# Kernel optimization log

Measured on AMD Instinct MI355X. Metric: run time of the kernel, lower is better.

The kernel has to match this reference:

```python
import jax, jax.numpy as jnp
import numpy as np

H = 8          # n_heads
THRESH = 0.5   # edge pruning threshold
LN_EPS = 1e-5


def setup_inputs() -> dict:
    key = jax.random.key(0)
    ks = jax.random.split(key, 24)
    B, S, D = 8, 128, 256
    N = S + 1
    hd = D // H

    def lin(k, fan_in, fan_out, gain=1.0):
        # xavier_uniform-ish init, stored as [in, out] (y = x @ W + b)
        lim = gain * np.sqrt(6.0 / (fan_in + fan_out))
        return jax.random.uniform(k, (fan_in, fan_out), jnp.float32, -lim, lim)

    g = 1.0 / np.sqrt(2.0)
    return {
        "desc": jax.random.normal(ks[0], (B, S, D), jnp.float32),
        "nv": jax.random.normal(ks[1], (B, N, D), jnp.float32),
        "W_gt": lin(ks[2], D, D), "b_gt": jnp.zeros((D,), jnp.float32),
        "topo_bias": jnp.zeros((1,), jnp.float32),
        "W_q": lin(ks[3], D, D, g), "b_q": jnp.zeros((D,), jnp.float32),
        "W_k": lin(ks[4], D, D, g), "b_k": jnp.zeros((D,), jnp.float32),
        "W_v": lin(ks[5], D, D, g), "b_v": jnp.zeros((D,), jnp.float32),
        "W_e1": lin(ks[6], 2 * D, D), "b_e1": jnp.zeros((D,), jnp.float32),
        "ln_g": jnp.ones((D,), jnp.float32), "ln_b": jnp.zeros((D,), jnp.float32),
        "W_e2": lin(ks[7], D, D), "b_e2": jnp.zeros((D,), jnp.float32),
        "w_attn": lin(ks[8], 3 * hd, 1, g)[:, 0], "b_attn": jnp.zeros((), jnp.float32),
        "W_o": lin(ks[9], D, D, g), "b_o": jnp.zeros((D,), jnp.float32),
    }


def _forward(desc, nv, W_gt, b_gt, topo_bias, W_q, b_q, W_k, b_k, W_v, b_v,
             W_e1, b_e1, ln_g, ln_b, W_e2, b_e2, w_attn, b_attn, W_o, b_o):
    B, N, D = nv.shape
    S = N - 1
    hd = D // H

    # 1. global topology
    d = desc @ W_gt + b_gt                                   # [B,S,D]
    dn = d / jnp.linalg.norm(d, axis=-1, keepdims=True)
    global_top = jax.nn.sigmoid(jnp.einsum('bid,bjd->bij', dn, dn) + topo_bias[0])

    # 2. sample-wise similarity
    var = nv[:, 1:, :]
    vn = var / jnp.linalg.norm(var, axis=-1, keepdims=True)
    sample_sim = jnp.einsum('bid,bjd->bij', vn, vn)
    adj_mat = global_top * sample_sim

    # 3. remove self-connection, squash
    diag_mask = 1.0 - jnp.eye(S, dtype=adj_mat.dtype)
    adj = jax.nn.sigmoid(adj_mat * diag_mask)

    # 4. straight-through edge pruning (frozen=False path)
    hard = (adj > THRESH).astype(adj.dtype)
    adj = hard - jax.lax.stop_gradient(adj) + adj

    # 5. edge attributes: Linear(concat(d_i,d_j)) decomposed into two matmuls
    a = d @ W_e1[:D]                                          # node_i part [B,S,D]
    b_ = d @ W_e1[D:]                                         # node_j part [B,S,D]
    pre = jnp.zeros((B, N, N, D), dtype=d.dtype)
    pre = pre.at[:, 1:, 1:].set(a[:, :, None, :] + b_[:, None, :, :])
    cls = a + b_                                              # concat(d_j,d_j) rows
    pre = pre.at[:, 0, 1:].set(cls).at[:, 1:, 0].set(cls)
    pre = pre + b_e1                                          # (0,0) entry = bias only (zeros input)
    mu = pre.mean(-1, keepdims=True)
    vr = ((pre - mu) ** 2).mean(-1, keepdims=True)
    e = jax.nn.relu((pre - mu) * jax.lax.rsqrt(vr + LN_EPS) * ln_g + ln_b)
    e = e @ W_e2 + b_e2                                       # [B,N,N,D]
    e = e.reshape(B, N, N, H, hd).transpose(0, 3, 1, 2, 4)    # [B,H,N,N,hd]

    # padded adjacency: CLS row attends to all vars, col 0 masked
    na = jnp.zeros((B, N, N), dtype=adj.dtype)
    na = na.at[:, 1:, 1:].set(adj).at[:, 0, 1:].set(1.0)
    e = e * na[:, None, :, :, None]

    # 6. additive attention: attn_proj(concat(q,k,e)) decomposed
    q = (nv @ W_q + b_q).reshape(B, N, H, hd).transpose(0, 2, 1, 3)
    k = (nv @ W_k + b_k).reshape(B, N, H, hd).transpose(0, 2, 1, 3)
    v = (nv @ W_v + b_v).reshape(B, N, H, hd).transpose(0, 2, 1, 3)
    wq, wk, we = w_attn[:hd], w_attn[hd:2 * hd], w_attn[2 * hd:]
    scores = (jnp.einsum('bhid,d->bhi', q, wq)[:, :, :, None]
              + jnp.einsum('bhjd,d->bhj', k, wk)[:, :, None, :]
              + jnp.einsum('bhijd,d->bhij', e, we) + b_attn)
    scores = scores + (na[:, None, :, :] == 0).astype(scores.dtype) * -1e9
    attn = jax.nn.softmax(scores, axis=-1)                    # dropout = identity (eval)

    ctx = jnp.einsum('bhij,bhjd->bhid', attn, v)
    out = ctx.transpose(0, 2, 1, 3).reshape(B, N, D) @ W_o + b_o
    return out, attn


def reference(desc, nv, W_gt, b_gt, topo_bias, W_q, b_q, W_k, b_k, W_v, b_v,
              W_e1, b_e1, ln_g, ln_b, W_e2, b_e2, w_attn, b_attn, W_o, b_o):
    return _forward(desc, nv, W_gt, b_gt, topo_bias, W_q, b_q, W_k, b_k, W_v, b_v,
                    W_e1, b_e1, ln_g, ln_b, W_e2, b_e2, w_attn, b_attn, W_o, b_o)
```

## Files before the change

### kernel.cpp

```cpp
#include <hip/hip_runtime.h>
#include <math.h>

#define BB 8
#define SS 128
#define NN 129
#define DD 256
#define HH 8
#define LN_EPS 1e-5f

#define OFF_A    0
#define OFF_BPT  262144
#define OFF_CPT  524288
#define OFF_VART 786432
#define OFF_V    1048576
#define OFF_SQ   1312768
#define OFF_SK   1321024
#define OFF_MA   1329280
#define OFF_QA   1330304
#define OFF_MB   1331328
#define OFF_QB   1332352
#define OFF_MC   1333376
#define OFF_QC   1334400
#define OFF_U    1335424
#define OFF_UB   1337472

struct SA {
    float dsc[4][DD];
    float drow[4][DD];
    float4 red[8][4][64];
    float part[24][4];
};
struct SB {
    float rows[2][DD];
    float4 redq[8][2][64];
    float4 redk[8][2][64];
};
union SMA { SA a; SB b; };

__global__ __launch_bounds__(512) void ka_all(
    const float* __restrict__ desc, const float* __restrict__ nv,
    const float* __restrict__ W_gt, const float* __restrict__ b_gt,
    const float* __restrict__ W_e1, const float* __restrict__ b_e1,
    const float* __restrict__ W_q, const float* __restrict__ b_q,
    const float* __restrict__ W_k, const float* __restrict__ b_k,
    const float* __restrict__ W_v, const float* __restrict__ b_v,
    const float* __restrict__ W_e2, const float* __restrict__ b_e2,
    const float* __restrict__ w_attn,
    float* __restrict__ a, float* __restrict__ bp_t, float* __restrict__ cp_t,
    float* __restrict__ var_t, float* __restrict__ v,
    float* __restrict__ sq, float* __restrict__ sk,
    float* __restrict__ ma, float* __restrict__ qa, float* __restrict__ mb,
    float* __restrict__ qb, float* __restrict__ mc, float* __restrict__ qc,
    float* __restrict__ U, float* __restrict__ ubias) {
    __shared__ SMA sm;
    const int bx = blockIdx.x, t = threadIdx.x;

    if (bx < 256) {
        SA& S = sm.a;
        const int b = bx >> 5, s0 = (bx & 31) * 4;
        const int dq = t & 63, kh = t >> 6;
        for (int e = t; e < 4 * DD; e += 512)
            S.dsc[e >> 8][e & 255] = desc[(size_t)(b * SS + s0 + (e >> 8)) * DD + (e & 255)];
        __syncthreads();
        {
            float4 acc[4];
#pragma unroll
            for (int r = 0; r < 4; r++) acc[r] = make_float4(0.f, 0.f, 0.f, 0.f);
            const int kb = kh * 32;
#pragma unroll 4
            for (int k = kb; k < kb + 32; k++) {
                float4 w = *(const float4*)&W_gt[k * DD + 4 * dq];
#pragma unroll
                for (int r = 0; r < 4; r++) {
                    float x = S.dsc[r][k];
                    acc[r].x = fmaf(x, w.x, acc[r].x); acc[r].y = fmaf(x, w.y, acc[r].y);
                    acc[r].z = fmaf(x, w.z, acc[r].z); acc[r].w = fmaf(x, w.w, acc[r].w);
                }
            }
#pragma unroll
            for (int r = 0; r < 4; r++) S.red[kh][r][dq] = acc[r];
        }
        __syncthreads();
        for (int e = t; e < 4 * DD; e += 512) {
            int r = e >> 8, d2 = e & 255;
            float s = b_gt[d2];
#pragma unroll
            for (int kk = 0; kk < 8; kk++) s += ((const float*)S.red[kk][r])[d2];
            S.drow[r][d2] = s;
        }
        __syncthreads();
        {
            float4 acc[4];
#pragma unroll
            for (int r = 0; r < 4; r++) acc[r] = make_float4(0.f, 0.f, 0.f, 0.f);
            const int kb = kh * 32;
#pragma unroll 4
            for (int k = kb; k < kb + 32; k++) {
                float4 w = *(const float4*)&W_e1[k * DD + 4 * dq];
#pragma unroll
                for (int r = 0; r < 4; r++) {
                    float x = S.drow[r][k];
                    acc[r].x = fmaf(x, w.x, acc[r].x); acc[r].y = fmaf(x, w.y, acc[r].y);
                    acc[r].z = fmaf(x, w.z, acc[r].z); acc[r].w = fmaf(x, w.w, acc[r].w);
                }
            }
#pragma unroll
            for (int r = 0; r < 4; r++) S.red[kh][r][dq] = acc[r];
        }
        __syncthreads();
        float avf[4];
        if (t < 256) {
            const int d2 = t;
#pragma unroll
            for (int r = 0; r < 4; r++) {
                float s = 0.f;
#pragma unroll
                for (int kk = 0; kk < 8; kk++) s += ((const float*)S.red[kk][r])[d2];
                avf[r] = s;
                a[(size_t)(b * SS + s0 + r) * DD + d2] = s;
            }
        }
        __syncthreads();
        {
            float4 acc[4];
#pragma unroll
            for (int r = 0; r < 4; r++) acc[r] = make_float4(0.f, 0.f, 0.f, 0.f);
            const int kb = kh * 32;
#pragma unroll 4
            for (int k = kb; k < kb + 32; k++) {
                float4 w = *(const float4*)&W_e1[(DD + k) * DD + 4 * dq];
#pragma unroll
                for (int r = 0; r < 4; r++) {
                    float x = S.drow[r][k];
                    acc[r].x = fmaf(x, w.x, acc[r].x); acc[r].y = fmaf(x, w.y, acc[r].y);
                    acc[r].z = fmaf(x, w.z, acc[r].z); acc[r].w = fmaf(x, w.w, acc[r].w);
                }
            }
#pragma unroll
            for (int r = 0; r < 4; r++) S.red[kh][r][dq] = acc[r];
        }
        __syncthreads();
        if (t < 256) {
            const int d2 = t;
            float bvf[4], cvf[4];
            float be1 = b_e1[d2];
#pragma unroll
            for (int r = 0; r < 4; r++) {
                float s = 0.f;
#pragma unroll
                for (int kk = 0; kk < 8; kk++) s += ((const float*)S.red[kk][r])[d2];
                bvf[r] = s + be1; cvf[r] = avf[r] + bvf[r];
            }
            float4 f4;
            f4.x = bvf[0]; f4.y = bvf[1]; f4.z = bvf[2]; f4.w = bvf[3];
            *(float4*)(bp_t + (size_t)(b * DD + d2) * SS + s0) = f4;
            f4.x = cvf[0]; f4.y = cvf[1]; f4.z = cvf[2]; f4.w = cvf[3];
            *(float4*)(cp_t + (size_t)(b * DD + d2) * SS + s0) = f4;
            float nvv[4];
#pragma unroll
            for (int r = 0; r < 4; r++) nvv[r] = nv[(size_t)(b * NN + 1 + s0 + r) * DD + d2];
            f4.x = nvv[0]; f4.y = nvv[1]; f4.z = nvv[2]; f4.w = nvv[3];
            *(float4*)(var_t + (size_t)(b * DD + d2) * SS + s0) = f4;
            float vals[24];
#pragma unroll
            for (int r = 0; r < 4; r++) {
                vals[r * 6 + 0] = avf[r]; vals[r * 6 + 1] = avf[r] * avf[r];
                vals[r * 6 + 2] = bvf[r]; vals[r * 6 + 3] = bvf[r] * bvf[r];
                vals[r * 6 + 4] = cvf[r]; vals[r * 6 + 5] = cvf[r] * cvf[r];
            }
            int lane = t & 63, wid = t >> 6;
#pragma unroll
            for (int vv = 0; vv < 24; vv++) {
                float x = vals[vv];
                for (int o = 32; o; o >>= 1) x += __shfl_xor(x, o, 64);
                if (lane == 0) S.part[vv][wid] = x;
            }
        }
        __syncthreads();
        if (t < 24) {
            float ssum = (S.part[t][0] + S.part[t][1]) + (S.part[t][2] + S.part[t][3]);
            int st = t % 6;
            int row = b * SS + s0 + t / 6;
            float m = ssum * (1.f / DD);
            float* dstp = (st == 0) ? ma : (st == 1) ? qa : (st == 2) ? mb
                         : (st == 3) ? qb : (st == 4) ? mc : qc;
            dstp[row] = m;
        }
    } else if (bx < 776) {
        SB& S = sm.b;
        const int idx = bx - 256;
        const int b = idx / 65, n0 = (idx % 65) * 2;
        const int dq = t & 63, kh = t >> 6;
        {
            int r = t >> 8, d2 = t & 255;
            int n = n0 + r; if (n >= NN) n = NN - 1;
            S.rows[r][d2] = nv[(size_t)(b * NN + n) * DD + d2];
        }
        __syncthreads();
        {
            float4 aq[2], ak[2];
#pragma unroll
            for (int r = 0; r < 2; r++) { aq[r] = make_float4(0.f, 0.f, 0.f, 0.f); ak[r] = aq[r]; }
            const int kb = kh * 32;
#pragma unroll 4
            for (int k = kb; k < kb + 32; k++) {
                float4 wq = *(const float4*)&W_q[k * DD + 4 * dq];
                float4 wk = *(const float4*)&W_k[k * DD + 4 * dq];
#pragma unroll
                for (int r = 0; r < 2; r++) {
                    float x = S.rows[r][k];
                    aq[r].x = fmaf(x, wq.x, aq[r].x); aq[r].y = fmaf(x, wq.y, aq[r].y);
                    aq[r].z = fmaf(x, wq.z, aq[r].z); aq[r].w = fmaf(x, wq.w, aq[r].w);
                    ak[r].x = fmaf(x, wk.x, ak[r].x); ak[r].y = fmaf(x, wk.y, ak[r].y);
                    ak[r].z = fmaf(x, wk.z, ak[r].z); ak[r].w = fmaf(x, wk.w, ak[r].w);
                }
            }
#pragma unroll
            for (int r = 0; r < 2; r++) { S.redq[kh][r][dq] = aq[r]; S.redk[kh][r][dq] = ak[r]; }
        }
        __syncthreads();
        {
            const int d2 = t & 255, r = t >> 8;
            const int n = n0 + r;
            float qf = b_q[d2], kf = b_k[d2];
#pragma unroll
            for (int kk = 0; kk < 8; kk++) {
                qf += ((const float*)S.redq[kk][r])[d2];
                kf += ((const float*)S.redk[kk][r])[d2];
            }
            float xq = qf * w_attn[d2 & 31];
            float xk = kf * w_attn[32 + (d2 & 31)];
#pragma unroll
            for (int o = 16; o; o >>= 1) { xq += __shfl_xor(xq, o, 32); xk += __shfl_xor(xk, o, 32); }
            if ((d2 & 31) == 0 && n < NN) {
                sq[(size_t)(b * HH + (d2 >> 5)) * NN + n] = xq;
                sk[(size_t)(b * HH + (d2 >> 5)) * NN + n] = xk;
            }
        }
        __syncthreads();
        {
            float4 av[2];
#pragma unroll
            for (int r = 0; r < 2; r++) av[r] = make_float4(0.f, 0.f, 0.f, 0.f);
            const int kb = kh * 32;
#pragma unroll 4
            for (int k = kb; k < kb + 32; k++) {
                float4 wv = *(const float4*)&W_v[k * DD + 4 * dq];
#pragma unroll
                for (int r = 0; r < 2; r++) {
                    float x = S.rows[r][k];
                    av[r].x = fmaf(x, wv.x, av[r].x); av[r].y = fmaf(x, wv.y, av[r].y);
                    av[r].z = fmaf(x, wv.z, av[r].z); av[r].w = fmaf(x, wv.w, av[r].w);
                }
            }
#pragma unroll
            for (int r = 0; r < 2; r++) S.redq[kh][r][dq] = av[r];
        }
        __syncthreads();
        {
            const int d2 = t & 255, r = t >> 8;
            const int n = n0 + r;
            if (n < NN) {
                float vf = b_v[d2];
#pragma unroll
                for (int kk = 0; kk < 8; kk++) vf += ((const float*)S.redq[kk][r])[d2];
                v[(size_t)(b * NN + n) * DD + d2] = vf;
            }
        }
    } else {
        const int ri = bx - 776;
        if (t < 256) {
            const int c = t;
            const float wec = w_attn[64 + (c & 31)];
#pragma unroll
            for (int rr = 0; rr < 4; rr++) {
                int r = ri * 4 + rr;
                float x = W_e2[(size_t)r * DD + c] * wec;
#pragma unroll
                for (int o = 16; o; o >>= 1) x += __shfl_xor(x, o, 32);
                if ((c & 31) == 0) U[r * HH + (c >> 5)] = x;
            }
            if (ri == 0) {
                float x = b_e2[c] * wec;
#pragma unroll
                for (int o = 16; o; o >>= 1) x += __shfl_xor(x, o, 32);
                if ((c & 31) == 0) ubias[c >> 5] = x;
            }
        }
    }
}

__global__ __launch_bounds__(256) void kmega(
    const float* __restrict__ a, const float* __restrict__ bp_t, const float* __restrict__ cp_t,
    const float* __restrict__ var_t, const float* __restrict__ nv,
    const float* __restrict__ v,
    const float* __restrict__ ma, const float* __restrict__ qa,
    const float* __restrict__ mb, const float* __restrict__ qb,
    const float* __restrict__ mc, const float* __restrict__ qc,
    const float* __restrict__ sq, const float* __restrict__ sk,
    const float* __restrict__ ln_g, const float* __restrict__ ln_b,
    const float* __restrict__ U, const float* __restrict__ ubias,
    const float* __restrict__ b_attn,
    const float* __restrict__ W_o, const float* __restrict__ b_o,
    float* __restrict__ attn, float* __restrict__ out) {
    const int it = blockIdx.x, b = blockIdx.y;
    const int i0 = it * 2;
    const int t = threadIdx.x;
    const int dg = t >> 6, jl = t & 63;
    __shared__ float Arow[2][DD];
    __shared__ float Vrow[2][DD];
    __shared__ __attribute__((aligned(8))) float2 lnsm[DD];
    __shared__ __attribute__((aligned(16))) float4 Usm[DD][2];
    __shared__ __attribute__((aligned(8))) float rsm[2][SS], nmm[2][SS], mkm[2][SS], pnm[2][SS];
    __shared__ float skm[HH * NN];
    __shared__ float sqb[2][HH], ubm[HH];
    __shared__ float sc[2][HH][NN + 3];
    __shared__ __attribute__((aligned(16))) float red[4][2][HH][SS];
    __shared__ float csm[2][DD];

    {
        int ic0 = i0, ic1 = (i0 + 1 < NN) ? i0 + 1 : NN - 1;
        Arow[0][t] = (ic0 >= 1) ? a[((size_t)b * SS + ic0 - 1) * DD + t] : 0.f;
        Arow[1][t] = (ic1 >= 1) ? a[((size_t)b * SS + ic1 - 1) * DD + t] : 0.f;
        Vrow[0][t] = nv[((size_t)b * NN + ic0) * DD + t];
        Vrow[1][t] = nv[((size_t)b * NN + ic1) * DD + t];
        float2 g; g.x = ln_g[t]; g.y = ln_b[t]; lnsm[t] = g;
        Usm[t][0] = *(const float4*)&U[t * HH];
        Usm[t][1] = *(const float4*)&U[t * HH + 4];
        for (int e = t; e < HH * NN; e += 256) skm[e] = sk[(size_t)b * HH * NN + e];
        if (t < 16) {
            int il = t >> 3, h = t & 7;
            int i = i0 + il; if (i > NN - 1) i = NN - 1;
            sqb[il][h] = sq[(size_t)b * HH * NN + h * NN + i] + b_attn[0];
        }
        if (t < HH) ubm[t] = ubias[t];
    }
    __syncthreads();

    {
        float cr[2][2] = {{0.f, 0.f}, {0.f, 0.f}}, dvv[2][2] = {{0.f, 0.f}, {0.f, 0.f}};
        const float* bc = bp_t + ((size_t)b * DD + dg * 64) * SS + 2 * jl;
        const float* vc = var_t + ((size_t)b * DD + dg * 64) * SS + 2 * jl;
#pragma unroll 4
        for (int dd = 0; dd < 64; dd++) {
            float2 bv = *(const float2*)(bc + (size_t)dd * SS);
            float2 vv = *(const float2*)(vc + (size_t)dd * SS);
            const int d = dg * 64 + dd;
            float A0 = Arow[0][d], A1 = Arow[1][d];
            float V0 = Vrow[0][d], V1 = Vrow[1][d];
            cr[0][0] = fmaf(A0, bv.x, cr[0][0]); cr[0][1] = fmaf(A0, bv.y, cr[0][1]);
            cr[1][0] = fmaf(A1, bv.x, cr[1][0]); cr[1][1] = fmaf(A1, bv.y, cr[1][1]);
            dvv[0][0] = fmaf(V0, vv.x, dvv[0][0]); dvv[0][1] = fmaf(V0, vv.y, dvv[0][1]);
            dvv[1][0] = fmaf(V1, vv.x, dvv[1][0]); dvv[1][1] = fmaf(V1, vv.y, dvv[1][1]);
        }
#pragma unroll
        for (int il = 0; il < 2; il++) {
            float2 w0; w0.x = cr[il][0]; w0.y = cr[il][1];
            float2 w1; w1.x = dvv[il][0]; w1.y = dvv[il][1];
            *(float2*)&red[dg][il][0][2 * jl] = w0;
            *(float2*)&red[dg][il][1][2 * jl] = w1;
        }
    }
    __syncthreads();
    if (t < SS) {
        const int j = t;
#pragma unroll
        for (int il = 0; il < 2; il++) {
            int i = i0 + il; if (i > NN - 1) i = NN - 1;
            float rs, nm, mk, pen;
            if (i == 0) {
                float mu = mc[b * SS + j], q2 = qc[b * SS + j];
                rs = rsqrtf(q2 - mu * mu + LN_EPS); nm = -mu * rs; mk = 1.f; pen = 0.f;
            } else {
                float cr = (red[0][il][0][j] + red[1][il][0][j]) + (red[2][il][0][j] + red[3][il][0][j]);
                float dv = (red[0][il][1][j] + red[1][il][1][j]) + (red[2][il][1][j] + red[3][il][1][j]);
                float muA = ma[b * SS + i - 1], qA = qa[b * SS + i - 1];
                float muB = mb[b * SS + j], qB = qb[b * SS + j];
                float mu = muA + muB;
                float var = qA + qB + 2.f * cr * (1.f / DD) - mu * mu;
                rs = rsqrtf(var + LN_EPS); nm = -mu * rs;
                mk = ((i - 1) != j && dv > 0.f) ? 1.f : 0.f;
                pen = (mk == 0.f) ? -1e9f : 0.f;
            }
            rsm[il][j] = rs; nmm[il][j] = nm; mkm[il][j] = mk; pnm[il][j] = pen;
        }
    }
    __syncthreads();
    float acc[2][HH][2];
#pragma unroll
    for (int il = 0; il < 2; il++)
#pragma unroll
        for (int h = 0; h < HH; h++) { acc[il][h][0] = 0.f; acc[il][h][1] = 0.f; }
    {
        const float* Bb = bp_t + ((size_t)b * DD + dg * 64) * SS + 2 * jl;
        float2 r0 = *(const float2*)&rsm[0][2 * jl];
        float2 n0 = *(const float2*)&nmm[0][2 * jl];
        float2 r1 = *(const float2*)&rsm[1][2 * jl];
        float2 n1 = *(const float2*)&nmm[1][2 * jl];
        if (i0 != 0) {
#pragma unroll 4
            for (int dd = 0; dd < 64; dd++) {
                const int d = dg * 64 + dd;
                float2 bv = *(const float2*)(Bb + (size_t)dd * SS);
                float A0 = Arow[0][d], A1 = Arow[1][d];
                float2 gb = lnsm[d];
                float4 u0 = Usm[d][0], u1 = Usm[d][1];
                float y0 = fmaf(A0 + bv.x, r0.x, n0.x); y0 = fmaf(y0, gb.x, gb.y);
                float y1 = fmaf(A0 + bv.y, r0.y, n0.y); y1 = fmaf(y1, gb.x, gb.y);
                float e0 = fmaxf(y0, 0.f), e1 = fmaxf(y1, 0.f);
                float z0 = fmaf(A1 + bv.x, r1.x, n1.x); z0 = fmaf(z0, gb.x, gb.y);
                float z1 = fmaf(A1 + bv.y, r1.y, n1.y); z1 = fmaf(z1, gb.x, gb.y);
                float f0 = fmaxf(z0, 0.f), f1 = fmaxf(z1, 0.f);
                acc[0][0][0] = fmaf(e0, u0.x, acc[0][0][0]); acc[0][0][1] = fmaf(e1, u0.x, acc[0][0][1]);
                acc[0][1][0] = fmaf(e0, u0.y, acc[0][1][0]); acc[0][1][1] = fmaf(e1, u0.y, acc[0][1][1]);
                acc[0][2][0] = fmaf(e0, u0.z, acc[0][2][0]); acc[0][2][1] = fmaf(e1, u0.z, acc[0][2][1]);
                acc[0][3][0] = fmaf(e0, u0.w, acc[0][3][0]); acc[0][3][1] = fmaf(e1, u0.w, acc[0][3][1]);
                acc[0][4][0] = fmaf(e0, u1.x, acc[0][4][0]); acc[0][4][1] = fmaf(e1, u1.x, acc[0][4][1]);
                acc[0][5][0] = fmaf(e0, u1.y, acc[0][5][0]); acc[0][5][1] = fmaf(e1, u1.y, acc[0][5][1]);
                acc[0][6][0] = fmaf(e0, u1.z, acc[0][6][0]); acc[0][6][1] = fmaf(e1, u1.z, acc[0][6][1]);
                acc[0][7][0] = fmaf(e0, u1.w, acc[0][7][0]); acc[0][7][1] = fmaf(e1, u1.w, acc[0][7][1]);
                acc[1][0][0] = fmaf(f0, u0.x, acc[1][0][0]); acc[1][0][1] = fmaf(f1, u0.x, acc[1][0][1]);
                acc[1][1][0] = fmaf(f0, u0.y, acc[1][1][0]); acc[1][1][1] = fmaf(f1, u0.y, acc[1][1][1]);
                acc[1][2][0] = fmaf(f0, u0.z, acc[1][2][0]); acc[1][2][1] = fmaf(f1, u0.z, acc[1][2][1]);
                acc[1][3][0] = fmaf(f0, u0.w, acc[1][3][0]); acc[1][3][1] = fmaf(f1, u0.w, acc[1][3][1]);
                acc[1][4][0] = fmaf(f0, u1.x, acc[1][4][0]); acc[1][4][1] = fmaf(f1, u1.x, acc[1][4][1]);
                acc[1][5][0] = fmaf(f0, u1.y, acc[1][5][0]); acc[1][5][1] = fmaf(f1, u1.y, acc[1][5][1]);
                acc[1][6][0] = fmaf(f0, u1.z, acc[1][6][0]); acc[1][6][1] = fmaf(f1, u1.z, acc[1][6][1]);
                acc[1][7][0] = fmaf(f0, u1.w, acc[1][7][0]); acc[1][7][1] = fmaf(f1, u1.w, acc[1][7][1]);
            }
        } else {
            const float* Bc = cp_t + ((size_t)b * DD + dg * 64) * SS + 2 * jl;
#pragma unroll 4
            for (int dd = 0; dd < 64; dd++) {
                const int d = dg * 64 + dd;
                float2 bA = *(const float2*)(Bc + (size_t)dd * SS);
                float2 bB = *(const float2*)(Bb + (size_t)dd * SS);
                float A0 = Arow[0][d], A1 = Arow[1][d];
                float2 gb = lnsm[d];
                float4 u0 = Usm[d][0], u1 = Usm[d][1];
                float y0 = fmaf(A0 + bA.x, r0.x, n0.x); y0 = fmaf(y0, gb.x, gb.y);
                float y1 = fmaf(A0 + bA.y, r0.y, n0.y); y1 = fmaf(y1, gb.x, gb.y);
                float e0 = fmaxf(y0, 0.f), e1 = fmaxf(y1, 0.f);
                float z0 = fmaf(A1 + bB.x, r1.x, n1.x); z0 = fmaf(z0, gb.x, gb.y);
                float z1 = fmaf(A1 + bB.y, r1.y, n1.y); z1 = fmaf(z1, gb.x, gb.y);
                float f0 = fmaxf(z0, 0.f), f1 = fmaxf(z1, 0.f);
                acc[0][0][0] = fmaf(e0, u0.x, acc[0][0][0]); acc[0][0][1] = fmaf(e1, u0.x, acc[0][0][1]);
                acc[0][1][0] = fmaf(e0, u0.y, acc[0][1][0]); acc[0][1][1] = fmaf(e1, u0.y, acc[0][1][1]);
                acc[0][2][0] = fmaf(e0, u0.z, acc[0][2][0]); acc[0][2][1] = fmaf(e1, u0.z, acc[0][2][1]);
                acc[0][3][0] = fmaf(e0, u0.w, acc[0][3][0]); acc[0][3][1] = fmaf(e1, u0.w, acc[0][3][1]);
                acc[0][4][0] = fmaf(e0, u1.x, acc[0][4][0]); acc[0][4][1] = fmaf(e1, u1.x, acc[0][4][1]);
                acc[0][5][0] = fmaf(e0, u1.y, acc[0][5][0]); acc[0][5][1] = fmaf(e1, u1.y, acc[0][5][1]);
                acc[0][6][0] = fmaf(e0, u1.z, acc[0][6][0]); acc[0][6][1] = fmaf(e1, u1.z, acc[0][6][1]);
                acc[0][7][0] = fmaf(e0, u1.w, acc[0][7][0]); acc[0][7][1] = fmaf(e1, u1.w, acc[0][7][1]);
                acc[1][0][0] = fmaf(f0, u0.x, acc[1][0][0]); acc[1][0][1] = fmaf(f1, u0.x, acc[1][0][1]);
                acc[1][1][0] = fmaf(f0, u0.y, acc[1][1][0]); acc[1][1][1] = fmaf(f1, u0.y, acc[1][1][1]);
                acc[1][2][0] = fmaf(f0, u0.z, acc[1][2][0]); acc[1][2][1] = fmaf(f1, u0.z, acc[1][2][1]);
                acc[1][3][0] = fmaf(f0, u0.w, acc[1][3][0]); acc[1][3][1] = fmaf(f1, u0.w, acc[1][3][1]);
                acc[1][4][0] = fmaf(f0, u1.x, acc[1][4][0]); acc[1][4][1] = fmaf(f1, u1.x, acc[1][4][1]);
                acc[1][5][0] = fmaf(f0, u1.y, acc[1][5][0]); acc[1][5][1] = fmaf(f1, u1.y, acc[1][5][1]);
                acc[1][6][0] = fmaf(f0, u1.z, acc[1][6][0]); acc[1][6][1] = fmaf(f1, u1.z, acc[1][6][1]);
                acc[1][7][0] = fmaf(f0, u1.w, acc[1][7][0]); acc[1][7][1] = fmaf(f1, u1.w, acc[1][7][1]);
            }
        }
    }
#pragma unroll
    for (int il = 0; il < 2; il++)
#pragma unroll
        for (int h = 0; h < HH; h++) {
            float2 w; w.x = acc[il][h][0]; w.y = acc[il][h][1];
            *(float2*)&red[dg][il][h][2 * jl] = w;
        }
    __syncthreads();
    for (int e = t; e < 2 * HH * SS; e += 256) {
        int il = e >> 10, h = (e >> 7) & 7, j = e & 127;
        float s = (red[0][il][h][j] + red[1][il][h][j]) + (red[2][il][h][j] + red[3][il][h][j]);
        sc[il][h][1 + j] = sqb[il][h] + skm[h * NN + 1 + j] + (s + ubm[h]) * mkm[il][j] + pnm[il][j];
    }
    if (t < 16) { int il = t >> 3, h = t & 7; sc[il][h][0] = sqb[il][h] + skm[h * NN] - 1e9f; }
    __syncthreads();
    {
        const int row = t >> 4, l = t & 15;
        const int il = row >> 3, h = row & 7;
        const int i = i0 + il;
        float m = -INFINITY;
        for (int j = l; j < NN; j += 16) m = fmaxf(m, sc[il][h][j]);
#pragma unroll
        for (int o = 8; o; o >>= 1) m = fmaxf(m, __shfl_xor(m, o, 16));
        float s = 0.f;
        float ev[9];
        int cnt = 0;
        for (int j = l; j < NN; j += 16) { float e = __expf(sc[il][h][j] - m); ev[cnt++] = e; s += e; }
#pragma unroll
        for (int o = 8; o; o >>= 1) s += __shfl_xor(s, o, 16);
        float inv = 1.f / s;
        float* arow = attn + (((size_t)b * HH + h) * NN + i) * NN;
        cnt = 0;
        for (int j = l; j < NN; j += 16) {
            float p = ev[cnt++] * inv;
            sc[il][h][j] = p;
            if (i < NN) arow[j] = p;
        }
    }
    __syncthreads();
    {
        const int dq = t & 63, jg = t >> 6;
        const int h = dq >> 3;
        float ca[2][4] = {{0.f, 0.f, 0.f, 0.f}, {0.f, 0.f, 0.f, 0.f}};
#pragma unroll 4
        for (int jj = 0; jj < 33; jj++) {
            int j = jg * 33 + jj;
            if (j < NN) {
                float4 vv = *(const float4*)&v[((size_t)b * NN + j) * DD + 4 * dq];
                float p0 = sc[0][h][j], p1 = sc[1][h][j];
                ca[0][0] = fmaf(p0, vv.x, ca[0][0]); ca[0][1] = fmaf(p0, vv.y, ca[0][1]);
                ca[0][2] = fmaf(p0, vv.z, ca[0][2]); ca[0][3] = fmaf(p0, vv.w, ca[0][3]);
                ca[1][0] = fmaf(p1, vv.x, ca[1][0]); ca[1][1] = fmaf(p1, vv.y, ca[1][1]);
                ca[1][2] = fmaf(p1, vv.z, ca[1][2]); ca[1][3] = fmaf(p1, vv.w, ca[1][3]);
            }
        }
        float* redf = &red[0][0][0][0];
#pragma unroll
        for (int il = 0; il < 2; il++) {
            float4 w; w.x = ca[il][0]; w.y = ca[il][1]; w.z = ca[il][2]; w.w = ca[il][3];
            *(float4*)&redf[jg * 512 + il * 256 + 4 * dq] = w;
        }
    }
    __syncthreads();
    {
        const float* redf = &red[0][0][0][0];
#pragma unroll
        for (int il = 0; il < 2; il++)
            csm[il][t] = (redf[il * 256 + t] + redf[512 + il * 256 + t])
                       + (redf[1024 + il * 256 + t] + redf[1536 + il * 256 + t]);
    }
    __syncthreads();
    {
        const int cq = t & 63, kg = t >> 6;
        float o[2][4] = {{0.f, 0.f, 0.f, 0.f}, {0.f, 0.f, 0.f, 0.f}};
#pragma unroll 4
        for (int kk = 0; kk < 64; kk++) {
            int k = kg * 64 + kk;
            float4 w = *(const float4*)&W_o[(size_t)k * DD + 4 * cq];
            float c0 = csm[0][k], c1 = csm[1][k];
            o[0][0] = fmaf(c0, w.x, o[0][0]); o[0][1] = fmaf(c0, w.y, o[0][1]);
            o[0][2] = fmaf(c0, w.z, o[0][2]); o[0][3] = fmaf(c0, w.w, o[0][3]);
            o[1][0] = fmaf(c1, w.x, o[1][0]); o[1][1] = fmaf(c1, w.y, o[1][1]);
            o[1][2] = fmaf(c1, w.z, o[1][2]); o[1][3] = fmaf(c1, w.w, o[1][3]);
        }
        float* redf = &red[0][0][0][0];
#pragma unroll
        for (int il = 0; il < 2; il++) {
            float4 w; w.x = o[il][0]; w.y = o[il][1]; w.z = o[il][2]; w.w = o[il][3];
            *(float4*)&redf[kg * 512 + il * 256 + 4 * cq] = w;
        }
    }
    __syncthreads();
    {
        const float* redf = &red[0][0][0][0];
        float bo = b_o[t];
#pragma unroll
        for (int il = 0; il < 2; il++) {
            int i = i0 + il;
            if (i < NN) {
                float s = (redf[il * 256 + t] + redf[512 + il * 256 + t])
                        + (redf[1024 + il * 256 + t] + redf[1536 + il * 256 + t]) + bo;
                out[((size_t)b * NN + i) * DD + t] = s;
            }
        }
    }
}

extern "C" void kernel_launch(void* const* d_in, const int* in_sizes, int n_in,
                              void* d_out, int out_size, void* d_ws, size_t ws_size,
                              hipStream_t stream) {
    const float* desc   = (const float*)d_in[0];
    const float* nv     = (const float*)d_in[1];
    const float* W_gt   = (const float*)d_in[2];
    const float* b_gt   = (const float*)d_in[3];
    const float* W_q    = (const float*)d_in[5];
    const float* b_q    = (const float*)d_in[6];
    const float* W_k    = (const float*)d_in[7];
    const float* b_k    = (const float*)d_in[8];
    const float* W_v    = (const float*)d_in[9];
    const float* b_v    = (const float*)d_in[10];
    const float* W_e1   = (const float*)d_in[11];
    const float* b_e1   = (const float*)d_in[12];
    const float* ln_g   = (const float*)d_in[13];
    const float* ln_b   = (const float*)d_in[14];
    const float* W_e2   = (const float*)d_in[15];
    const float* b_e2   = (const float*)d_in[16];
    const float* w_attn = (const float*)d_in[17];
    const float* b_attn = (const float*)d_in[18];
    const float* W_o    = (const float*)d_in[19];
    const float* b_o    = (const float*)d_in[20];

    float* ws   = (float*)d_ws;
    float* a    = ws + OFF_A;
    float* bp_t = ws + OFF_BPT;
    float* cp_t = ws + OFF_CPT;
    float* vart = ws + OFF_VART;
    float* v    = ws + OFF_V;
    float* sq   = ws + OFF_SQ;
    float* sk   = ws + OFF_SK;
    float* ma   = ws + OFF_MA;
    float* qa   = ws + OFF_QA;
    float* mb   = ws + OFF_MB;
    float* qb   = ws + OFF_QB;
    float* mc   = ws + OFF_MC;
    float* qc   = ws + OFF_QC;
    float* U    = ws + OFF_U;
    float* ub   = ws + OFF_UB;

    float* out  = (float*)d_out;
    float* attn = (float*)d_out + (size_t)BB * NN * DD;

    ka_all<<<dim3(840), dim3(512), 0, stream>>>(
        desc, nv, W_gt, b_gt, W_e1, b_e1, W_q, b_q, W_k, b_k, W_v, b_v,
        W_e2, b_e2, w_attn,
        a, bp_t, cp_t, vart, v, sq, sk, ma, qa, mb, qb, mc, qc, U, ub);
    kmega<<<dim3(65, BB), dim3(256), 0, stream>>>(
        a, bp_t, cp_t, vart, nv, v, ma, qa, mb, qb, mc, qc, sq, sk,
        ln_g, ln_b, U, ub, b_attn, W_o, b_o, attn, out);
}
```

Baseline: 191.2 us.

## Reduce across d-groups with wavefront shuffles and shrink shared memory via unions

The thread mapping changes so the four d-groups of each column pair sit inside one 64-lane wavefront. Partial sums are then combined with __shfl_xor instead of being written to a 4x2x8x128 shared reduction buffer. The big red array is replaced by smaller unions that reuse storage for Vrow/csm and the reduction stages, cutting LDS per block and one sync-plus-reduce pass. The cost is that global loads are now less contiguous per wavefront (16 lanes per row segment), and only a quarter of lanes do the score writes.

```diff
diff --git a/kernel.cpp b/kernel.cpp
--- a/kernel.cpp
+++ b/kernel.cpp
@@ -290,7 +290,7 @@
     }
 }
 
-__global__ __launch_bounds__(256) void kmega(
+__global__ __launch_bounds__(256) void kmega2(
     const float* __restrict__ a, const float* __restrict__ bp_t, const float* __restrict__ cp_t,
     const float* __restrict__ var_t, const float* __restrict__ nv,
     const float* __restrict__ v,
@@ -306,24 +306,29 @@
     const int it = blockIdx.x, b = blockIdx.y;
     const int i0 = it * 2;
     const int t = threadIdx.x;
-    const int dg = t >> 6, jl = t & 63;
+    const int w = t >> 6, l = t & 63;
+    const int dgp = l >> 4;
+    const int jp = w * 16 + (l & 15);
+
     __shared__ float Arow[2][DD];
-    __shared__ float Vrow[2][DD];
     __shared__ __attribute__((aligned(8))) float2 lnsm[DD];
     __shared__ __attribute__((aligned(16))) float4 Usm[DD][2];
     __shared__ __attribute__((aligned(8))) float rsm[2][SS], nmm[2][SS], mkm[2][SS], pnm[2][SS];
     __shared__ float skm[HH * NN];
     __shared__ float sqb[2][HH], ubm[HH];
     __shared__ float sc[2][HH][NN + 3];
-    __shared__ __attribute__((aligned(16))) float red[4][2][HH][SS];
-    __shared__ float csm[2][DD];
+    __shared__ union { float Vrow[2][DD]; float csm[2][DD]; } uv;
+    __shared__ __attribute__((aligned(16))) union {
+        struct { float crs[2][SS]; float dvs[2][SS]; } p1;
+        float redc[4][2][DD];
+    } ur;
 
     {
         int ic0 = i0, ic1 = (i0 + 1 < NN) ? i0 + 1 : NN - 1;
         Arow[0][t] = (ic0 >= 1) ? a[((size_t)b * SS + ic0 - 1) * DD + t] : 0.f;
         Arow[1][t] = (ic1 >= 1) ? a[((size_t)b * SS + ic1 - 1) * DD + t] : 0.f;
-        Vrow[0][t] = nv[((size_t)b * NN + ic0) * DD + t];
-        Vrow[1][t] = nv[((size_t)b * NN + ic1) * DD + t];
+        uv.Vrow[0][t] = nv[((size_t)b * NN + ic0) * DD + t];
+        uv.Vrow[1][t] = nv[((size_t)b * NN + ic1) * DD + t];
         float2 g; g.x = ln_g[t]; g.y = ln_b[t]; lnsm[t] = g;
         Usm[t][0] = *(const float4*)&U[t * HH];
         Usm[t][1] = *(const float4*)&U[t * HH + 4];
@@ -339,26 +344,37 @@
 
     {
         float cr[2][2] = {{0.f, 0.f}, {0.f, 0.f}}, dvv[2][2] = {{0.f, 0.f}, {0.f, 0.f}};
-        const float* bc = bp_t + ((size_t)b * DD + dg * 64) * SS + 2 * jl;
-        const float* vc = var_t + ((size_t)b * DD + dg * 64) * SS + 2 * jl;
+        const float* bc = bp_t + ((size_t)b * DD + dgp * 64) * SS + 2 * jp;
+        const float* vc = var_t + ((size_t)b * DD + dgp * 64) * SS + 2 * jp;
 #pragma unroll 4
         for (int dd = 0; dd < 64; dd++) {
             float2 bv = *(const float2*)(bc + (size_t)dd * SS);
             float2 vv = *(const float2*)(vc + (size_t)dd * SS);
-            const int d = dg * 64 + dd;
+            const int d = dgp * 64 + dd;
             float A0 = Arow[0][d], A1 = Arow[1][d];
-            float V0 = Vrow[0][d], V1 = Vrow[1][d];
+            float V0 = uv.Vrow[0][d], V1 = uv.Vrow[1][d];
             cr[0][0] = fmaf(A0, bv.x, cr[0][0]); cr[0][1] = fmaf(A0, bv.y, cr[0][1]);
             cr[1][0] = fmaf(A1, bv.x, cr[1][0]); cr[1][1] = fmaf(A1, bv.y, cr[1][1]);
             dvv[0][0] = fmaf(V0, vv.x, dvv[0][0]); dvv[0][1] = fmaf(V0, vv.y, dvv[0][1]);
             dvv[1][0] = fmaf(V1, vv.x, dvv[1][0]); dvv[1][1] = fmaf(V1, vv.y, dvv[1][1]);
         }
 #pragma unroll
-        for (int il = 0; il < 2; il++) {
-            float2 w0; w0.x = cr[il][0]; w0.y = cr[il][1];
-            float2 w1; w1.x = dvv[il][0]; w1.y = dvv[il][1];
-            *(float2*)&red[dg][il][0][2 * jl] = w0;
-            *(float2*)&red[dg][il][1][2 * jl] = w1;
+        for (int il = 0; il < 2; il++)
+#pragma unroll
+            for (int jj = 0; jj < 2; jj++) {
+                float c = cr[il][jj], d2 = dvv[il][jj];
+                c += __shfl_xor(c, 16); c += __shfl_xor(c, 32);
+                d2 += __shfl_xor(d2, 16); d2 += __shfl_xor(d2, 32);
+                cr[il][jj] = c; dvv[il][jj] = d2;
+            }
+        if (l < 16) {
+#pragma unroll
+            for (int il = 0; il < 2; il++) {
+                float2 wc; wc.x = cr[il][0]; wc.y = cr[il][1];
+                float2 wd; wd.x = dvv[il][0]; wd.y = dvv[il][1];
+                *(float2*)&ur.p1.crs[il][2 * jp] = wc;
+                *(float2*)&ur.p1.dvs[il][2 * jp] = wd;
+            }
         }
     }
     __syncthreads();
@@ -372,8 +388,8 @@
                 float mu = mc[b * SS + j], q2 = qc[b * SS + j];
                 rs = rsqrtf(q2 - mu * mu + LN_EPS); nm = -mu * rs; mk = 1.f; pen = 0.f;
             } else {
-                float cr = (red[0][il][0][j] + red[1][il][0][j]) + (red[2][il][0][j] + red[3][il][0][j]);
-                float dv = (red[0][il][1][j] + red[1][il][1][j]) + (red[2][il][1][j] + red[3][il][1][j]);
+                float cr = ur.p1.crs[il][j];
+                float dv = ur.p1.dvs[il][j];
                 float muA = ma[b * SS + i - 1], qA = qa[b * SS + i - 1];
                 float muB = mb[b * SS + j], qB = qb[b * SS + j];
                 float mu = muA + muB;
@@ -392,15 +408,15 @@
 #pragma unroll
         for (int h = 0; h < HH; h++) { acc[il][h][0] = 0.f; acc[il][h][1] = 0.f; }
     {
-        const float* Bb = bp_t + ((size_t)b * DD + dg * 64) * SS + 2 * jl;
-        float2 r0 = *(const float2*)&rsm[0][2 * jl];
-        float2 n0 = *(const float2*)&nmm[0][2 * jl];
-        float2 r1 = *(const float2*)&rsm[1][2 * jl];
-        float2 n1 = *(const float2*)&nmm[1][2 * jl];
+        const float* Bb = bp_t + ((size_t)b * DD + dgp * 64) * SS + 2 * jp;
+        float2 r0 = *(const float2*)&rsm[0][2 * jp];
+        float2 n0 = *(const float2*)&nmm[0][2 * jp];
+        float2 r1 = *(const float2*)&rsm[1][2 * jp];
+        float2 n1 = *(const float2*)&nmm[1][2 * jp];
         if (i0 != 0) {
 #pragma unroll 4
             for (int dd = 0; dd < 64; dd++) {
-                const int d = dg * 64 + dd;
+                const int d = dgp * 64 + dd;
                 float2 bv = *(const float2*)(Bb + (size_t)dd * SS);
                 float A0 = Arow[0][d], A1 = Arow[1][d];
                 float2 gb = lnsm[d];
@@ -429,10 +445,10 @@
                 acc[1][7][0] = fmaf(f0, u1.w, acc[1][7][0]); acc[1][7][1] = fmaf(f1, u1.w, acc[1][7][1]);
             }
         } else {
-            const float* Bc = cp_t + ((size_t)b * DD + dg * 64) * SS + 2 * jl;
+            const float* Bc = cp_t + ((size_t)b * DD + dgp * 64) * SS + 2 * jp;
 #pragma unroll 4
             for (int dd = 0; dd < 64; dd++) {
-                const int d = dg * 64 + dd;
+                const int d = dgp * 64 + dd;
                 float2 bA = *(const float2*)(Bc + (size_t)dd * SS);
                 float2 bB = *(const float2*)(Bb + (size_t)dd * SS);
                 float A0 = Arow[0][d], A1 = Arow[1][d];
@@ -467,35 +483,44 @@
     for (int il = 0; il < 2; il++)
 #pragma unroll
         for (int h = 0; h < HH; h++) {
-            float2 w; w.x = acc[il][h][0]; w.y = acc[il][h][1];
-            *(float2*)&red[dg][il][h][2 * jl] = w;
-        }
-    __syncthreads();
-    for (int e = t; e < 2 * HH * SS; e += 256) {
-        int il = e >> 10, h = (e >> 7) & 7, j = e & 127;
-        float s = (red[0][il][h][j] + red[1][il][h][j]) + (red[2][il][h][j] + red[3][il][h][j]);
-        sc[il][h][1 + j] = sqb[il][h] + skm[h * NN + 1 + j] + (s + ubm[h]) * mkm[il][j] + pnm[il][j];
+            float s0 = acc[il][h][0], s1 = acc[il][h][1];
+            s0 += __shfl_xor(s0, 16); s0 += __shfl_xor(s0, 32);
+            s1 += __shfl_xor(s1, 16); s1 += __shfl_xor(s1, 32);
+            acc[il][h][0] = s0; acc[il][h][1] = s1;
+        }
+    if (l < 16) {
+        const int j0 = 2 * jp, j1 = j0 + 1;
+#pragma unroll
+        for (int il = 0; il < 2; il++) {
+            float mk0 = mkm[il][j0], pn0 = pnm[il][j0];
+            float mk1 = mkm[il][j1], pn1 = pnm[il][j1];
+#pragma unroll
+            for (int h = 0; h < HH; h++) {
+                sc[il][h][1 + j0] = sqb[il][h] + skm[h * NN + 1 + j0] + (acc[il][h][0] + ubm[h]) * mk0 + pn0;
+                sc[il][h][1 + j1] = sqb[il][h] + skm[h * NN + 1 + j1] + (acc[il][h][1] + ubm[h]) * mk1 + pn1;
+            }
+        }
     }
     if (t < 16) { int il = t >> 3, h = t & 7; sc[il][h][0] = sqb[il][h] + skm[h * NN] - 1e9f; }
     __syncthreads();
     {
-        const int row = t >> 4, l = t & 15;
+        const int row = t >> 4, ll = t & 15;
         const int il = row >> 3, h = row & 7;
         const int i = i0 + il;
         float m = -INFINITY;
-        for (int j = l; j < NN; j += 16) m = fmaxf(m, sc[il][h][j]);
+        for (int j = ll; j < NN; j += 16) m = fmaxf(m, sc[il][h][j]);
 #pragma unroll
         for (int o = 8; o; o >>= 1) m = fmaxf(m, __shfl_xor(m, o, 16));
         float s = 0.f;
         float ev[9];
         int cnt = 0;
-        for (int j = l; j < NN; j += 16) { float e = __expf(sc[il][h][j] - m); ev[cnt++] = e; s += e; }
+        for (int j = ll; j < NN; j += 16) { float e = __expf(sc[il][h][j] - m); ev[cnt++] = e; s += e; }
 #pragma unroll
         for (int o = 8; o; o >>= 1) s += __shfl_xor(s, o, 16);
         float inv = 1.f / s;
         float* arow = attn + (((size_t)b * HH + h) * NN + i) * NN;
         cnt = 0;
-        for (int j = l; j < NN; j += 16) {
+        for (int j = ll; j < NN; j += 16) {
             float p = ev[cnt++] * inv;
             sc[il][h][j] = p;
             if (i < NN) arow[j] = p;
@@ -518,21 +543,17 @@
                 ca[1][2] = fmaf(p1, vv.z, ca[1][2]); ca[1][3] = fmaf(p1, vv.w, ca[1][3]);
             }
         }
-        float* redf = &red[0][0][0][0];
 #pragma unroll
         for (int il = 0; il < 2; il++) {
-            float4 w; w.x = ca[il][0]; w.y = ca[il][1]; w.z = ca[il][2]; w.w = ca[il][3];
-            *(float4*)&redf[jg * 512 + il * 256 + 4 * dq] = w;
-        }
-    }
-    __syncthreads();
-    {
-        const float* redf = &red[0][0][0][0];
-#pragma unroll
-        for (int il = 0; il < 2; il++)
-            csm[il][t] = (redf[il * 256 + t] + redf[512 + il * 256 + t])
-                       + (redf[1024 + il * 256 + t] + redf[1536 + il * 256 + t]);
-    }
+            float4 wv; wv.x = ca[il][0]; wv.y = ca[il][1]; wv.z = ca[il][2]; wv.w = ca[il][3];
+            *(float4*)&ur.redc[jg][il][4 * dq] = wv;
+        }
+    }
+    __syncthreads();
+#pragma unroll
+    for (int il = 0; il < 2; il++)
+        uv.csm[il][t] = (ur.redc[0][il][t] + ur.redc[1][il][t])
+                      + (ur.redc[2][il][t] + ur.redc[3][il][t]);
     __syncthreads();
     {
         const int cq = t & 63, kg = t >> 6;
@@ -540,30 +561,29 @@
 #pragma unroll 4
         for (int kk = 0; kk < 64; kk++) {
             int k = kg * 64 + kk;
-            float4 w = *(const float4*)&W_o[(size_t)k * DD + 4 * cq];
-            float c0 = csm[0][k], c1 = csm[1][k];
-            o[0][0] = fmaf(c0, w.x, o[0][0]); o[0][1] = fmaf(c0, w.y, o[0][1]);
-            o[0][2] = fmaf(c0, w.z, o[0][2]); o[0][3] = fmaf(c0, w.w, o[0][3]);
-            o[1][0] = fmaf(c1, w.x, o[1][0]); o[1][1] = fmaf(c1, w.y, o[1][1]);
-            o[1][2] = fmaf(c1, w.z, o[1][2]); o[1][3] = fmaf(c1, w.w, o[1][3]);
-        }
-        float* redf = &red[0][0][0][0];
+            float4 wv = *(const float4*)&W_o[(size_t)k * DD + 4 * cq];
+            float c0 = uv.csm[0][k], c1 = uv.csm[1][k];
+            o[0][0] = fmaf(c0, wv.x, o[0][0]); o[0][1] = fmaf(c0, wv.y, o[0][1]);
+            o[0][2] = fmaf(c0, wv.z, o[0][2]); o[0][3] = fmaf(c0, wv.w, o[0][3]);
+            o[1][0] = fmaf(c1, wv.x, o[1][0]); o[1][1] = fmaf(c1, wv.y, o[1][1]);
+            o[1][2] = fmaf(c1, wv.z, o[1][2]); o[1][3] = fmaf(c1, wv.w, o[1][3]);
+        }
+        __syncthreads();
 #pragma unroll
         for (int il = 0; il < 2; il++) {
-            float4 w; w.x = o[il][0]; w.y = o[il][1]; w.z = o[il][2]; w.w = o[il][3];
-            *(float4*)&redf[kg * 512 + il * 256 + 4 * cq] = w;
+            float4 wv; wv.x = o[il][0]; wv.y = o[il][1]; wv.z = o[il][2]; wv.w = o[il][3];
+            *(float4*)&ur.redc[kg][il][4 * cq] = wv;
         }
     }
     __syncthreads();
     {
-        const float* redf = &red[0][0][0][0];
         float bo = b_o[t];
 #pragma unroll
         for (int il = 0; il < 2; il++) {
             int i = i0 + il;
             if (i < NN) {
-                float s = (redf[il * 256 + t] + redf[512 + il * 256 + t])
-                        + (redf[1024 + il * 256 + t] + redf[1536 + il * 256 + t]) + bo;
+                float s = (ur.redc[0][il][t] + ur.redc[1][il][t])
+                        + (ur.redc[2][il][t] + ur.redc[3][il][t]) + bo;
                 out[((size_t)b * NN + i) * DD + t] = s;
             }
         }
@@ -618,7 +638,7 @@
         desc, nv, W_gt, b_gt, W_e1, b_e1, W_q, b_q, W_k, b_k, W_v, b_v,
         W_e2, b_e2, w_attn,
         a, bp_t, cp_t, vart, v, sq, sk, ma, qa, mb, qb, mc, qc, U, ub);
-    kmega<<<dim3(65, BB), dim3(256), 0, stream>>>(
+    kmega2<<<dim3(65, BB), dim3(256), 0, stream>>>(
         a, bp_t, cp_t, vart, nv, v, ma, qa, mb, qb, mc, qc, sq, sk,
         ln_g, ln_b, U, ub, b_attn, W_o, b_o, attn, out);
 }
```

Result: faster. 174.7 us (median of 2 runs) (-8.6%).
